# Kernel tuning notes

Measured on AMD Instinct MI355X. Metric: run time of the kernel, lower is better.

The kernel has to match this reference:

```python
import jax, jax.numpy as jnp
import numpy as np

B, S, D, H = 2, 2048, 768, 12
HD = D // H


def setup_inputs() -> dict:
    key = jax.random.key(0)
    ks = jax.random.split(key, 8)
    scale = 1.0 / np.sqrt(D)
    inp = {
        "q": jax.random.normal(ks[0], (B, S, D), jnp.float32),
        "k": jax.random.normal(ks[1], (B, S, D), jnp.float32),
        "v": jax.random.normal(ks[2], (B, S, D), jnp.float32),
        # causal mask: 1.0 where attention is disallowed (upper triangle)
        "mask": jnp.triu(jnp.ones((S, S), jnp.float32), k=1)[None, None, :, :],
        "Wq": jax.random.normal(ks[3], (D, D), jnp.float32) * scale,
        "bq": jnp.zeros((D,), jnp.float32),
        "Wk": jax.random.normal(ks[4], (D, D), jnp.float32) * scale,
        "bk": jnp.zeros((D,), jnp.float32),
        "Wv": jax.random.normal(ks[5], (D, D), jnp.float32) * scale,
        "bv": jnp.zeros((D,), jnp.float32),
        "Wo": jax.random.normal(ks[6], (D, D), jnp.float32) * scale,
        "bo": jnp.zeros((D,), jnp.float32),
    }
    return inp


def _split_heads(x):
    # [B, S, D] -> [B, H, S, HD]
    b, s, _ = x.shape
    return x.reshape(b, s, H, HD).transpose(0, 2, 1, 3)


def reference(q, k, v, mask, Wq, bq, Wk, bk, Wv, bv, Wo, bo):
    qh = _split_heads(q @ Wq + bq)
    kh = _split_heads(k @ Wk + bk)
    vh = _split_heads(v @ Wv + bv)
    scale = 1.0 / jnp.sqrt(jnp.asarray(HD, qh.dtype))
    # [B, H, Sq, Sk] — full attention matrix, as in the original
    scores = jnp.einsum("bhqd,bhkd->bhqk", qh, kh) * scale
    scores = scores + mask * -1e9
    attn = jax.nn.softmax(scores, axis=-1)  # dropout is identity at inference
    out = jnp.einsum("bhqk,bhkd->bhqd", attn, vh)
    out = out.transpose(0, 2, 1, 3).reshape(q.shape[0], -1, D)
    return out @ Wo + bo
```

## Files before the change

kernel.cpp:

```cpp
#include <hip/hip_runtime.h>

#define SEQ    2048
#define NB     2
#define DMODEL 768
#define NH     12
#define HDIM   64
#define BS     (NB * SEQ)

typedef __bf16  bf16x8  __attribute__((ext_vector_type(8)));
typedef ushort  ushort8 __attribute__((ext_vector_type(8)));
typedef float   floatx4 __attribute__((ext_vector_type(4)));

#define GLOBAL_AS __attribute__((address_space(1)))
#define LDS_AS    __attribute__((address_space(3)))

union PackU8 { ushort u[8]; uint4 v; };
union PackU4 { ushort u[4]; uint2 v; };

__device__ __forceinline__ ushort f2bf(float x) {
    union { float f; unsigned u; } t; t.f = x;
    unsigned r = t.u + 0x7fffu + ((t.u >> 16) & 1u);
    return (ushort)(r >> 16);
}

__device__ __forceinline__ bf16x8 ld_frag(const ushort* p) {
    return __builtin_bit_cast(bf16x8, *(const ushort8*)p);
}

__global__ void convert_x(const float* __restrict__ q, const float* __restrict__ k,
                          const float* __restrict__ v,
                          ushort* __restrict__ qo, ushort* __restrict__ ko,
                          ushort* __restrict__ vo)
{
    const float* src = blockIdx.z == 0 ? q : blockIdx.z == 1 ? k : v;
    ushort*      dst = blockIdx.z == 0 ? qo : blockIdx.z == 1 ? ko : vo;
    const int i = (blockIdx.x * 256 + threadIdx.x) * 4;
    const float4 f = *(const float4*)(src + i);
    ushort4 o;
    o.x = f2bf(f.x); o.y = f2bf(f.y); o.z = f2bf(f.z); o.w = f2bf(f.w);
    *(ushort4*)(dst + i) = o;
}

__global__ __launch_bounds__(256)
void convert_wT(const float* __restrict__ wq, const float* __restrict__ wk,
                const float* __restrict__ wv, const float* __restrict__ wo,
                ushort* __restrict__ wtcat, ushort* __restrict__ wto)
{
    __shared__ float Tf[64][69];
    const int z = blockIdx.z;
    const float* w = z == 0 ? wq : z == 1 ? wk : z == 2 ? wv : wo;
    ushort*      o = z < 3 ? wtcat + (size_t)z * DMODEL * DMODEL : wto;
    const int k0 = blockIdx.x * 64, n0 = blockIdx.y * 64;
    const int tid = threadIdx.x;
#pragma unroll
    for (int p = 0; p < 4; ++p) {
        const int idx = tid + p * 256;
        const int r = idx >> 4, c = (idx & 15) * 4;
        const float4 f = *(const float4*)&w[(size_t)(k0 + r) * DMODEL + n0 + c];
        Tf[r][c] = f.x; Tf[r][c + 1] = f.y; Tf[r][c + 2] = f.z; Tf[r][c + 3] = f.w;
    }
    __syncthreads();
#pragma unroll
    for (int p = 0; p < 2; ++p) {
        const int idx = tid + p * 256;
        const int n = idx >> 3, kk = (idx & 7) * 8;
        PackU8 pk;
#pragma unroll
        for (int j = 0; j < 8; ++j) pk.u[j] = f2bf(Tf[kk + j][n]);
        *(uint4*)&o[(size_t)(n0 + n) * DMODEL + k0 + kk] = pk.v;
    }
}

__global__ __launch_bounds__(256)
void gemm_qkv(const ushort* __restrict__ xq, const ushort* __restrict__ xk,
              const ushort* __restrict__ xv, const ushort* __restrict__ WT,
              const float* __restrict__ bq, const float* __restrict__ bk,
              const float* __restrict__ bv,
              ushort* __restrict__ oq, ushort* __restrict__ ok,
              ushort* __restrict__ ov)
{
    __shared__ __align__(16) ushort As[128 * 32];
    __shared__ __align__(16) ushort Bs[128 * 32];

    const int z = blockIdx.y / 6;
    const ushort* X = z == 0 ? xq : z == 1 ? xk : xv;

    const int tid  = threadIdx.x;
    const int lane = tid & 63;
    const int w    = tid >> 6;
    const int l15  = lane & 15;
    const int quad = lane >> 4;
    const int wm   = (w >> 1) * 64;
    const int wn   = (w & 1) * 64;
    const int row0 = blockIdx.x * 128;
    const int col0 = blockIdx.y * 128;

    floatx4 acc[4][4];
    const floatx4 fzero = {0.f, 0.f, 0.f, 0.f};
#pragma unroll
    for (int i = 0; i < 4; ++i)
#pragma unroll
        for (int j = 0; j < 4; ++j) acc[i][j] = fzero;

    const int rin = lane >> 2;
    const int gc  = (lane & 3) * 8;

    for (int k0 = 0; k0 < DMODEL; k0 += 32) {
#pragma unroll
        for (int p = 0; p < 2; ++p) {
            const int ch = w * 2 + p;
            const int r  = ch * 16 + rin;
            __builtin_amdgcn_global_load_lds(
                (const GLOBAL_AS uint*)&X[(size_t)(row0 + r) * DMODEL + k0 + gc],
                (LDS_AS uint*)&As[ch * 512], 16, 0, 0);
            __builtin_amdgcn_global_load_lds(
                (const GLOBAL_AS uint*)&WT[(size_t)(col0 + r) * DMODEL + k0 + gc],
                (LDS_AS uint*)&Bs[ch * 512], 16, 0, 0);
        }
        __syncthreads();

        bf16x8 af[4], bfr[4];
#pragma unroll
        for (int t = 0; t < 4; ++t) {
            af[t]  = ld_frag(&As[(wm + t * 16 + l15) * 32 + quad * 8]);
            bfr[t] = ld_frag(&Bs[(wn + t * 16 + l15) * 32 + quad * 8]);
        }
#pragma unroll
        for (int ti = 0; ti < 4; ++ti)
#pragma unroll
            for (int tj = 0; tj < 4; ++tj)
                acc[ti][tj] = __builtin_amdgcn_mfma_f32_16x16x32_bf16(
                    af[ti], bfr[tj], acc[ti][tj], 0, 0, 0);
        __syncthreads();
    }

    const int c0 = (blockIdx.y % 6) * 128;
    const float*  bias = z == 0 ? bq : z == 1 ? bk : bv;
    ushort*       out  = z == 0 ? oq : z == 1 ? ok : ov;
#pragma unroll
    for (int tj = 0; tj < 4; ++tj) {
        const int c_l = c0 + wn + tj * 16 + l15;
        const float bb = bias[c_l];
        const int h  = c_l >> 6;
        const int dd = c_l & 63;
#pragma unroll
        for (int ti = 0; ti < 4; ++ti) {
#pragma unroll
            for (int ri = 0; ri < 4; ++ri) {
                const int r_g = row0 + wm + ti * 16 + quad * 4 + ri;
                const int b   = r_g >> 11;
                const int s   = r_g & (SEQ - 1);
                out[(((size_t)(b * NH + h) * SEQ + s) << 6) + dd] =
                    f2bf(acc[ti][tj][ri] + bb);
            }
        }
    }
}

__global__ __launch_bounds__(256)
void gemm_out(const ushort* __restrict__ X, const ushort* __restrict__ WT,
              const float* __restrict__ bias, float* __restrict__ fo)
{
    __shared__ __align__(16) ushort As[64][40];
    __shared__ __align__(16) ushort Bs[128][40];

    const int tid  = threadIdx.x;
    const int lane = tid & 63;
    const int wv   = tid >> 6;
    const int wm   = (wv >> 1) * 32;
    const int wn   = (wv & 1) * 64;
    const int l15  = lane & 15;
    const int quad = lane >> 4;
    const int row0 = blockIdx.x * 64;
    const int col0 = blockIdx.y * 128;

    floatx4 acc[2][4];
    const floatx4 fzero = {0.f, 0.f, 0.f, 0.f};
#pragma unroll
    for (int i = 0; i < 2; ++i)
#pragma unroll
        for (int j = 0; j < 4; ++j) acc[i][j] = fzero;

    const int sr = tid >> 2;
    const int sc = (tid & 3) * 8;

    for (int k0 = 0; k0 < DMODEL; k0 += 32) {
        *(uint4*)&As[sr][sc] = *(const uint4*)&X[(size_t)(row0 + sr) * DMODEL + k0 + sc];
#pragma unroll
        for (int p = 0; p < 2; ++p) {
            const int r = sr + p * 64;
            *(uint4*)&Bs[r][sc] = *(const uint4*)&WT[(size_t)(col0 + r) * DMODEL + k0 + sc];
        }
        __syncthreads();

        bf16x8 af[2], bfr[4];
#pragma unroll
        for (int t = 0; t < 2; ++t)
            af[t] = ld_frag(&As[wm + t * 16 + l15][quad * 8]);
#pragma unroll
        for (int t = 0; t < 4; ++t)
            bfr[t] = ld_frag(&Bs[wn + t * 16 + l15][quad * 8]);
#pragma unroll
        for (int ti = 0; ti < 2; ++ti)
#pragma unroll
            for (int tj = 0; tj < 4; ++tj)
                acc[ti][tj] = __builtin_amdgcn_mfma_f32_16x16x32_bf16(
                    af[ti], bfr[tj], acc[ti][tj], 0, 0, 0);
        __syncthreads();
    }

#pragma unroll
    for (int tj = 0; tj < 4; ++tj) {
        const int c_g = col0 + wn + tj * 16 + l15;
        const float bb = bias[c_g];
#pragma unroll
        for (int ti = 0; ti < 2; ++ti)
#pragma unroll
            for (int ri = 0; ri < 4; ++ri) {
                const int r_g = row0 + wm + ti * 16 + quad * 4 + ri;
                fo[(size_t)r_g * DMODEL + c_g] = acc[ti][tj][ri] + bb;
            }
    }
}

__global__ void transpose_v(const ushort* __restrict__ vh, ushort* __restrict__ vt)
{
    __shared__ __align__(16) ushort T[64][72];
    const int bh = blockIdx.y;
    const int s0 = blockIdx.x * 64;
    const ushort* src = vh + (size_t)bh * SEQ * HDIM;
    ushort*       dst = vt + (size_t)bh * HDIM * SEQ;

#pragma unroll
    for (int p = 0; p < 2; ++p) {
        const int idx = threadIdx.x + p * 256;
        const int r = idx >> 3, c = (idx & 7) * 8;
        *(uint4*)&T[r][c] = *(const uint4*)&src[(size_t)(s0 + r) * HDIM + c];
    }
    __syncthreads();
#pragma unroll
    for (int p = 0; p < 2; ++p) {
        const int idx = threadIdx.x + p * 256;
        const int d = idx >> 3, c = (idx & 7) * 8;
        PackU8 pk;
#pragma unroll
        for (int j = 0; j < 8; ++j) pk.u[j] = T[c + j][d];
        *(uint4*)&dst[(size_t)d * SEQ + s0 + c] = pk.v;
    }
}

#define APAD 88

__device__ __forceinline__ void attn_epilogue(ushort* __restrict__ ctx, int b, int h,
                                              int qtile, int wv, int quad, int l15,
                                              const floatx4* O, float l)
{
    const float inv = 1.f / l;
    float ib[4];
#pragma unroll
    for (int ri = 0; ri < 4; ++ri) ib[ri] = __shfl(inv, quad * 4 + ri);
#pragma unroll
    for (int dj = 0; dj < 4; ++dj)
#pragma unroll
        for (int ri = 0; ri < 4; ++ri) {
            const int row = qtile * 32 + wv * 16 + quad * 4 + ri;
            ctx[((size_t)b * SEQ + row) * DMODEL + h * HDIM + dj * 16 + l15] =
                f2bf(O[dj][ri] * ib[ri]);
        }
}

__global__ __launch_bounds__(128)
void attn_mfma(const ushort* __restrict__ qh, const ushort* __restrict__ kh,
               const ushort* __restrict__ vt, ushort* __restrict__ ctx)
{
    __shared__ __align__(16) ushort Ks[2][64][APAD];
    __shared__ __align__(16) ushort Vs[2][64][APAD];
    __shared__ __align__(16) ushort Ps[32][APAD];

    const int tid  = threadIdx.x;
    const int lane = tid & 63;
    const int wv   = tid >> 6;
    const int l15  = lane & 15;
    const int quad = lane >> 4;
    const int id  = blockIdx.x;
    const int xcd = id & 7;
    const int jj  = id >> 3;
    const int g   = jj >> 5;
    const int x   = jj & 31;
    const int bh  = xcd + 8 * g;
    const int b   = bh / NH, h = bh - b * NH;
    const int qA  = x, qB = 63 - x;
    const int nkA = (qA >> 1) + 1;
    const size_t base = (size_t)bh * SEQ * HDIM;

    const float SCL = 0.125f * 1.44269504f;

    bf16x8 qfA[2], qfB[2];
#pragma unroll
    for (int ks = 0; ks < 2; ++ks) {
        qfA[ks] = ld_frag(&qh[base + (size_t)(qA * 32 + wv * 16 + l15) * HDIM + ks * 32 + quad * 8]);
        qfB[ks] = ld_frag(&qh[base + (size_t)(qB * 32 + wv * 16 + l15) * HDIM + ks * 32 + quad * 8]);
    }

    const int sr = tid >> 3;
    const int sc = (tid & 7) * 8;

    uint4 kreg[4], vreg[4];
#pragma unroll
    for (int p = 0; p < 4; ++p) {
        const int r = sr + p * 16;
        kreg[p] = *(const uint4*)&kh[base + (size_t)r * HDIM + sc];
        vreg[p] = *(const uint4*)&vt[base + (size_t)r * SEQ + sc];
    }
#pragma unroll
    for (int p = 0; p < 4; ++p) {
        const int r = sr + p * 16;
        *(uint4*)&Ks[0][r][sc] = kreg[p];
        *(uint4*)&Vs[0][r][sc] = vreg[p];
    }

    float l = 0.f;
    floatx4 O[4];
    const floatx4 fzero = {0.f, 0.f, 0.f, 0.f};
#pragma unroll
    for (int dj = 0; dj < 4; ++dj) O[dj] = fzero;

    const int rowA = qA * 32 + wv * 16 + l15;
    const int rowB = qB * 32 + wv * 16 + l15;

    for (int t = 0; t <= 32; ++t) {
        __syncthreads();
        const int buf = t & 1;

        if (t < 32) {
            const int kn  = (t + 1 < nkA) ? (t + 1) : (t + 1 - nkA);
            const int c0n = kn * 64;
#pragma unroll
            for (int p = 0; p < 4; ++p) {
                const int r = sr + p * 16;
                kreg[p] = *(const uint4*)&kh[base + (size_t)(c0n + r) * HDIM + sc];
                vreg[p] = *(const uint4*)&vt[base + (size_t)r * SEQ + c0n + sc];
            }
        }

        const bool isA   = (t < nkA);
        const int  kt    = isA ? t : t - nkA;
        const int  c0    = kt * 64;
        const bool diag  = (t == nkA - 1) || (t == 32);
        const int  row_g = isA ? rowA : rowB;

        floatx4 S[4];
#pragma unroll
        for (int nj = 0; nj < 4; ++nj) {
            S[nj] = fzero;
#pragma unroll
            for (int ks = 0; ks < 2; ++ks) {
                const bf16x8 kf = ld_frag(&Ks[buf][nj * 16 + l15][ks * 32 + quad * 8]);
                const bf16x8 qf = isA ? qfA[ks] : qfB[ks];
                S[nj] = __builtin_amdgcn_mfma_f32_16x16x32_bf16(kf, qf, S[nj], 0, 0, 0);
            }
        }

        float rs = 0.f;
#pragma unroll
        for (int nj = 0; nj < 4; ++nj) {
            PackU4 pk;
#pragma unroll
            for (int ri = 0; ri < 4; ++ri) {
                float p = __builtin_amdgcn_exp2f(S[nj][ri] * SCL);
                if (diag && (c0 + nj * 16 + quad * 4 + ri > row_g)) p = 0.f;
                rs += p;
                union { float f; unsigned u; } tb; tb.f = p;
                pk.u[ri] = (ushort)(tb.u >> 16);
            }
            *(uint2*)&Ps[wv * 16 + l15][nj * 16 + quad * 4] = pk.v;
        }
        rs += __shfl_xor(rs, 16);
        rs += __shfl_xor(rs, 32);
        l += rs;

        bf16x8 pf[2];
#pragma unroll
        for (int ks = 0; ks < 2; ++ks)
            pf[ks] = ld_frag(&Ps[wv * 16 + l15][ks * 32 + quad * 8]);
#pragma unroll
        for (int dj = 0; dj < 4; ++dj)
#pragma unroll
            for (int ks = 0; ks < 2; ++ks) {
                const bf16x8 vfr = ld_frag(&Vs[buf][dj * 16 + l15][ks * 32 + quad * 8]);
                O[dj] = __builtin_amdgcn_mfma_f32_16x16x32_bf16(pf[ks], vfr, O[dj], 0, 0, 0);
            }

        if (t == nkA - 1) {
            attn_epilogue(ctx, b, h, qA, wv, quad, l15, O, l);
            l = 0.f;
#pragma unroll
            for (int dj = 0; dj < 4; ++dj) O[dj] = fzero;
        }

        if (t < 32) {
#pragma unroll
            for (int p = 0; p < 4; ++p) {
                const int r = sr + p * 16;
                *(uint4*)&Ks[buf ^ 1][r][sc] = kreg[p];
                *(uint4*)&Vs[buf ^ 1][r][sc] = vreg[p];
            }
        }
    }

    attn_epilogue(ctx, b, h, qB, wv, quad, l15, O, l);
}

extern "C" void kernel_launch(void* const* d_in, const int* in_sizes, int n_in,
                              void* d_out, int out_size, void* d_ws, size_t ws_size,
                              hipStream_t stream)
{
    const float* q  = (const float*)d_in[0];
    const float* k  = (const float*)d_in[1];
    const float* v  = (const float*)d_in[2];
    const float* Wq = (const float*)d_in[4];
    const float* bq = (const float*)d_in[5];
    const float* Wk = (const float*)d_in[6];
    const float* bk = (const float*)d_in[7];
    const float* Wv = (const float*)d_in[8];
    const float* bv = (const float*)d_in[9];
    const float* Wo = (const float*)d_in[10];
    const float* bo = (const float*)d_in[11];
    float* out = (float*)d_out;

    char* ws = (char*)d_ws;
    const size_t ACT = (size_t)BS * DMODEL * 2;
    ushort* qx    = (ushort*)(ws);
    ushort* kx    = (ushort*)(ws + ACT);
    ushort* vx    = (ushort*)(ws + 2 * ACT);
    ushort* qhp   = (ushort*)(ws + 3 * ACT);
    ushort* khp   = (ushort*)(ws + 4 * ACT);
    ushort* vhp   = (ushort*)(ws + 5 * ACT);
    ushort* wtcat = (ushort*)(ws + 6 * ACT);
    ushort* wto   = wtcat + (size_t)3 * DMODEL * DMODEL;
    ushort* vhT   = vx;
    ushort* ctx   = qx;

    convert_x<<<dim3(BS * DMODEL / 1024, 1, 3), 256, 0, stream>>>(q, k, v, qx, kx, vx);
    convert_wT<<<dim3(12, 12, 4), 256, 0, stream>>>(Wq, Wk, Wv, Wo, wtcat, wto);
    gemm_qkv<<<dim3(BS / 128, 18), 256, 0, stream>>>(
        qx, kx, vx, wtcat, bq, bk, bv, qhp, khp, vhp);
    transpose_v<<<dim3(SEQ / 64, NB * NH), 256, 0, stream>>>(vhp, vhT);
    attn_mfma<<<dim3(768), 128, 0, stream>>>(qhp, khp, vhT, ctx);
    gemm_out<<<dim3(BS / 64, DMODEL / 128), 256, 0, stream>>>(ctx, wto, bo, out);
}
```

Measured before the change: 206.9 us.

## Use single-wave attention blocks with direct global-to-LDS async loads and swizzled LDS

The attention kernel moves from two waves to one wave per block, with each wave handling both 16-row halves of a 32-row query tile. K/V staging now uses global_load_lds straight into XOR-swizzled unpadded LDS, which removes the register round trip and the block barriers. Fragments are preloaded before the next stage is issued, and the MFMA sections get raised scheduling priority. The softmax scale times log2(e) is folded into the Q projection epilogue, so the per-element multiply in attention goes away. The trade is fewer threads per block and more registers per wave, which may reduce latency hiding.

```diff
diff --git a/kernel.cpp b/kernel.cpp
--- a/kernel.cpp
+++ b/kernel.cpp
@@ -137,6 +137,7 @@
     const int c0 = (blockIdx.y % 6) * 128;
     const float*  bias = z == 0 ? bq : z == 1 ? bk : bv;
     ushort*       out  = z == 0 ? oq : z == 1 ? ok : ov;
+    const float   sc   = (z == 0) ? 0.18033688f : 1.f;
 #pragma unroll
     for (int tj = 0; tj < 4; ++tj) {
         const int c_l = c0 + wn + tj * 16 + l15;
@@ -151,7 +152,7 @@
                 const int b   = r_g >> 11;
                 const int s   = r_g & (SEQ - 1);
                 out[(((size_t)(b * NH + h) * SEQ + s) << 6) + dd] =
-                    f2bf(acc[ti][tj][ri] + bb);
+                    f2bf((acc[ti][tj][ri] + bb) * sc);
             }
         }
     }
@@ -249,39 +250,19 @@
     }
 }
 
-#define APAD 88
-
-__device__ __forceinline__ void attn_epilogue(ushort* __restrict__ ctx, int b, int h,
-                                              int qtile, int wv, int quad, int l15,
-                                              const floatx4* O, float l)
-{
-    const float inv = 1.f / l;
-    float ib[4];
-#pragma unroll
-    for (int ri = 0; ri < 4; ++ri) ib[ri] = __shfl(inv, quad * 4 + ri);
-#pragma unroll
-    for (int dj = 0; dj < 4; ++dj)
-#pragma unroll
-        for (int ri = 0; ri < 4; ++ri) {
-            const int row = qtile * 32 + wv * 16 + quad * 4 + ri;
-            ctx[((size_t)b * SEQ + row) * DMODEL + h * HDIM + dj * 16 + l15] =
-                f2bf(O[dj][ri] * ib[ri]);
-        }
-}
-
-__global__ __launch_bounds__(128)
+__global__ __launch_bounds__(64)
 void attn_mfma(const ushort* __restrict__ qh, const ushort* __restrict__ kh,
                const ushort* __restrict__ vt, ushort* __restrict__ ctx)
 {
-    __shared__ __align__(16) ushort Ks[2][64][APAD];
-    __shared__ __align__(16) ushort Vs[2][64][APAD];
-    __shared__ __align__(16) ushort Ps[32][APAD];
-
-    const int tid  = threadIdx.x;
-    const int lane = tid & 63;
-    const int wv   = tid >> 6;
+    __shared__ __align__(16) ushort Ks[2][64][64];
+    __shared__ __align__(16) ushort Vs[2][64][64];
+    __shared__ __align__(16) ushort Ps[32][64];
+
+    const int lane = threadIdx.x;
     const int l15  = lane & 15;
     const int quad = lane >> 4;
+    const int e3   = l15 & 7;
+
     const int id  = blockIdx.x;
     const int xcd = id & 7;
     const int jj  = id >> 3;
@@ -293,122 +274,153 @@
     const int nkA = (qA >> 1) + 1;
     const size_t base = (size_t)bh * SEQ * HDIM;
 
-    const float SCL = 0.125f * 1.44269504f;
-
-    bf16x8 qfA[2], qfB[2];
+    bf16x8 qA0[2], qA1[2], qB0[2], qB1[2];
 #pragma unroll
     for (int ks = 0; ks < 2; ++ks) {
-        qfA[ks] = ld_frag(&qh[base + (size_t)(qA * 32 + wv * 16 + l15) * HDIM + ks * 32 + quad * 8]);
-        qfB[ks] = ld_frag(&qh[base + (size_t)(qB * 32 + wv * 16 + l15) * HDIM + ks * 32 + quad * 8]);
-    }
-
-    const int sr = tid >> 3;
-    const int sc = (tid & 7) * 8;
-
-    uint4 kreg[4], vreg[4];
-#pragma unroll
-    for (int p = 0; p < 4; ++p) {
-        const int r = sr + p * 16;
-        kreg[p] = *(const uint4*)&kh[base + (size_t)r * HDIM + sc];
-        vreg[p] = *(const uint4*)&vt[base + (size_t)r * SEQ + sc];
-    }
-#pragma unroll
-    for (int p = 0; p < 4; ++p) {
-        const int r = sr + p * 16;
-        *(uint4*)&Ks[0][r][sc] = kreg[p];
-        *(uint4*)&Vs[0][r][sc] = vreg[p];
-    }
-
-    float l = 0.f;
-    floatx4 O[4];
+        qA0[ks] = ld_frag(&qh[base + (size_t)(qA * 32 +      l15) * HDIM + ks * 32 + quad * 8]);
+        qA1[ks] = ld_frag(&qh[base + (size_t)(qA * 32 + 16 + l15) * HDIM + ks * 32 + quad * 8]);
+        qB0[ks] = ld_frag(&qh[base + (size_t)(qB * 32 +      l15) * HDIM + ks * 32 + quad * 8]);
+        qB1[ks] = ld_frag(&qh[base + (size_t)(qB * 32 + 16 + l15) * HDIM + ks * 32 + quad * 8]);
+    }
+
+    const int sr8  = lane >> 3;
+    const int kcol = ((lane & 7) ^ sr8) * 8;
+
+    auto stage = [&](int bufi, int c0s) {
+#pragma unroll
+        for (int p = 0; p < 8; ++p) {
+            __builtin_amdgcn_global_load_lds(
+                (const GLOBAL_AS uint*)&kh[base + (size_t)(c0s + 8 * p + sr8) * HDIM + kcol],
+                (LDS_AS uint*)&Ks[bufi][8 * p][0], 16, 0, 0);
+            __builtin_amdgcn_global_load_lds(
+                (const GLOBAL_AS uint*)&vt[base + (size_t)(8 * p + sr8) * SEQ + c0s + kcol],
+                (LDS_AS uint*)&Vs[bufi][8 * p][0], 16, 0, 0);
+        }
+    };
+
+    stage(0, 0);
+
+    float l0 = 0.f, l1 = 0.f;
+    floatx4 O[4][2];
     const floatx4 fzero = {0.f, 0.f, 0.f, 0.f};
 #pragma unroll
-    for (int dj = 0; dj < 4; ++dj) O[dj] = fzero;
-
-    const int rowA = qA * 32 + wv * 16 + l15;
-    const int rowB = qB * 32 + wv * 16 + l15;
+    for (int dj = 0; dj < 4; ++dj) { O[dj][0] = fzero; O[dj][1] = fzero; }
+
+    auto epilogue = [&](int qt) {
+        const float i0 = 1.f / l0, i1 = 1.f / l1;
+        float ib0[4], ib1[4];
+#pragma unroll
+        for (int ri = 0; ri < 4; ++ri) {
+            ib0[ri] = __shfl(i0, quad * 4 + ri);
+            ib1[ri] = __shfl(i1, quad * 4 + ri);
+        }
+#pragma unroll
+        for (int dj = 0; dj < 4; ++dj)
+#pragma unroll
+            for (int ri = 0; ri < 4; ++ri) {
+                const int r0 = qt * 32 + quad * 4 + ri;
+                ctx[((size_t)b * SEQ + r0) * DMODEL + h * HDIM + dj * 16 + l15] =
+                    f2bf(O[dj][0][ri] * ib0[ri]);
+                ctx[((size_t)b * SEQ + r0 + 16) * DMODEL + h * HDIM + dj * 16 + l15] =
+                    f2bf(O[dj][1][ri] * ib1[ri]);
+            }
+    };
+
+    asm volatile("s_waitcnt vmcnt(0)" ::: "memory");
 
     for (int t = 0; t <= 32; ++t) {
-        __syncthreads();
-        const int buf = t & 1;
+        const int  cur  = t & 1;
+        const bool isA  = (t < nkA);
+        const int  kt   = isA ? t : t - nkA;
+        const int  c0   = kt * 64;
+        const bool diag = (t == nkA - 1) || (t == 32);
+        const int  qt   = isA ? qA : qB;
+
+        bf16x8 kf[4][2], vf[4][2];
+#pragma unroll
+        for (int nj = 0; nj < 4; ++nj)
+#pragma unroll
+            for (int ks = 0; ks < 2; ++ks) {
+                kf[nj][ks] = ld_frag(&Ks[cur][nj * 16 + l15][(ks * 32 + quad * 8) ^ (e3 << 3)]);
+                vf[nj][ks] = ld_frag(&Vs[cur][nj * 16 + l15][(ks * 32 + quad * 8) ^ (e3 << 3)]);
+            }
 
         if (t < 32) {
-            const int kn  = (t + 1 < nkA) ? (t + 1) : (t + 1 - nkA);
-            const int c0n = kn * 64;
-#pragma unroll
-            for (int p = 0; p < 4; ++p) {
-                const int r = sr + p * 16;
-                kreg[p] = *(const uint4*)&kh[base + (size_t)(c0n + r) * HDIM + sc];
-                vreg[p] = *(const uint4*)&vt[base + (size_t)r * SEQ + c0n + sc];
-            }
-        }
-
-        const bool isA   = (t < nkA);
-        const int  kt    = isA ? t : t - nkA;
-        const int  c0    = kt * 64;
-        const bool diag  = (t == nkA - 1) || (t == 32);
-        const int  row_g = isA ? rowA : rowB;
-
-        floatx4 S[4];
+            const int kn = (t + 1 < nkA) ? (t + 1) : (t + 1 - nkA);
+            stage(cur ^ 1, kn * 64);
+        }
+
+        const bf16x8 q0k0 = isA ? qA0[0] : qB0[0];
+        const bf16x8 q0k1 = isA ? qA0[1] : qB0[1];
+        const bf16x8 q1k0 = isA ? qA1[0] : qB1[0];
+        const bf16x8 q1k1 = isA ? qA1[1] : qB1[1];
+
+        floatx4 S[4][2];
+        __builtin_amdgcn_s_setprio(1);
 #pragma unroll
         for (int nj = 0; nj < 4; ++nj) {
-            S[nj] = fzero;
+            S[nj][0] = __builtin_amdgcn_mfma_f32_16x16x32_bf16(kf[nj][0], q0k0, fzero, 0, 0, 0);
+            S[nj][1] = __builtin_amdgcn_mfma_f32_16x16x32_bf16(kf[nj][0], q1k0, fzero, 0, 0, 0);
+            S[nj][0] = __builtin_amdgcn_mfma_f32_16x16x32_bf16(kf[nj][1], q0k1, S[nj][0], 0, 0, 0);
+            S[nj][1] = __builtin_amdgcn_mfma_f32_16x16x32_bf16(kf[nj][1], q1k1, S[nj][1], 0, 0, 0);
+        }
+        __builtin_amdgcn_s_setprio(0);
+
+        float rs0 = 0.f, rs1 = 0.f;
+        const int rg0 = qt * 32 + l15;
+#pragma unroll
+        for (int nj = 0; nj < 4; ++nj) {
+            PackU4 p0, p1;
+#pragma unroll
+            for (int ri = 0; ri < 4; ++ri) {
+                const int krow = c0 + nj * 16 + quad * 4 + ri;
+                float v0 = __builtin_amdgcn_exp2f(S[nj][0][ri]);
+                float v1 = __builtin_amdgcn_exp2f(S[nj][1][ri]);
+                if (diag) {
+                    if (krow > rg0)      v0 = 0.f;
+                    if (krow > rg0 + 16) v1 = 0.f;
+                }
+                rs0 += v0; rs1 += v1;
+                union { float f; unsigned u; } t0, t1;
+                t0.f = v0; t1.f = v1;
+                p0.u[ri] = (ushort)(t0.u >> 16);
+                p1.u[ri] = (ushort)(t1.u >> 16);
+            }
+            *(uint2*)&Ps[l15     ][(nj * 16 + quad * 4) ^ (e3 << 3)] = p0.v;
+            *(uint2*)&Ps[16 + l15][(nj * 16 + quad * 4) ^ (e3 << 3)] = p1.v;
+        }
+        rs0 += __shfl_xor(rs0, 16); rs0 += __shfl_xor(rs0, 32);
+        rs1 += __shfl_xor(rs1, 16); rs1 += __shfl_xor(rs1, 32);
+        l0 += rs0; l1 += rs1;
+
+        bf16x8 pf0[2], pf1[2];
+#pragma unroll
+        for (int ks = 0; ks < 2; ++ks) {
+            pf0[ks] = ld_frag(&Ps[l15     ][(ks * 32 + quad * 8) ^ (e3 << 3)]);
+            pf1[ks] = ld_frag(&Ps[16 + l15][(ks * 32 + quad * 8) ^ (e3 << 3)]);
+        }
+
+        __builtin_amdgcn_s_setprio(1);
+#pragma unroll
+        for (int dj = 0; dj < 4; ++dj)
 #pragma unroll
             for (int ks = 0; ks < 2; ++ks) {
-                const bf16x8 kf = ld_frag(&Ks[buf][nj * 16 + l15][ks * 32 + quad * 8]);
-                const bf16x8 qf = isA ? qfA[ks] : qfB[ks];
-                S[nj] = __builtin_amdgcn_mfma_f32_16x16x32_bf16(kf, qf, S[nj], 0, 0, 0);
-            }
-        }
-
-        float rs = 0.f;
-#pragma unroll
-        for (int nj = 0; nj < 4; ++nj) {
-            PackU4 pk;
-#pragma unroll
-            for (int ri = 0; ri < 4; ++ri) {
-                float p = __builtin_amdgcn_exp2f(S[nj][ri] * SCL);
-                if (diag && (c0 + nj * 16 + quad * 4 + ri > row_g)) p = 0.f;
-                rs += p;
-                union { float f; unsigned u; } tb; tb.f = p;
-                pk.u[ri] = (ushort)(tb.u >> 16);
-            }
-            *(uint2*)&Ps[wv * 16 + l15][nj * 16 + quad * 4] = pk.v;
-        }
-        rs += __shfl_xor(rs, 16);
-        rs += __shfl_xor(rs, 32);
-        l += rs;
-
-        bf16x8 pf[2];
-#pragma unroll
-        for (int ks = 0; ks < 2; ++ks)
-            pf[ks] = ld_frag(&Ps[wv * 16 + l15][ks * 32 + quad * 8]);
-#pragma unroll
-        for (int dj = 0; dj < 4; ++dj)
-#pragma unroll
-            for (int ks = 0; ks < 2; ++ks) {
-                const bf16x8 vfr = ld_frag(&Vs[buf][dj * 16 + l15][ks * 32 + quad * 8]);
-                O[dj] = __builtin_amdgcn_mfma_f32_16x16x32_bf16(pf[ks], vfr, O[dj], 0, 0, 0);
-            }
+                O[dj][0] = __builtin_amdgcn_mfma_f32_16x16x32_bf16(pf0[ks], vf[dj][ks], O[dj][0], 0, 0, 0);
+                O[dj][1] = __builtin_amdgcn_mfma_f32_16x16x32_bf16(pf1[ks], vf[dj][ks], O[dj][1], 0, 0, 0);
+            }
+        __builtin_amdgcn_s_setprio(0);
 
         if (t == nkA - 1) {
-            attn_epilogue(ctx, b, h, qA, wv, quad, l15, O, l);
-            l = 0.f;
-#pragma unroll
-            for (int dj = 0; dj < 4; ++dj) O[dj] = fzero;
-        }
-
-        if (t < 32) {
-#pragma unroll
-            for (int p = 0; p < 4; ++p) {
-                const int r = sr + p * 16;
-                *(uint4*)&Ks[buf ^ 1][r][sc] = kreg[p];
-                *(uint4*)&Vs[buf ^ 1][r][sc] = vreg[p];
-            }
-        }
-    }
-
-    attn_epilogue(ctx, b, h, qB, wv, quad, l15, O, l);
+            epilogue(qA);
+            l0 = 0.f; l1 = 0.f;
+#pragma unroll
+            for (int dj = 0; dj < 4; ++dj) { O[dj][0] = fzero; O[dj][1] = fzero; }
+        }
+
+        asm volatile("s_waitcnt vmcnt(0)" ::: "memory");
+    }
+
+    epilogue(qB);
 }
 
 extern "C" void kernel_launch(void* const* d_in, const int* in_sizes, int n_in,
@@ -446,6 +458,6 @@
     gemm_qkv<<<dim3(BS / 128, 18), 256, 0, stream>>>(
         qx, kx, vx, wtcat, bq, bk, bv, qhp, khp, vhp);
     transpose_v<<<dim3(SEQ / 64, NB * NH), 256, 0, stream>>>(vhp, vhT);
-    attn_mfma<<<dim3(768), 128, 0, stream>>>(qhp, khp, vhT, ctx);
+    attn_mfma<<<dim3(768), 64, 0, stream>>>(qhp, khp, vhT, ctx);
     gemm_out<<<dim3(BS / 64, DMODEL / 128), 256, 0, stream>>>(ctx, wto, bo, out);
 }
```

Measured after the change: 210.9 us. About the same (+1.9%).
